# Kernel tuning notes

Measured on AMD Instinct MI355X. Metric: run time of the kernel, lower is better.

The kernel has to match this reference:

```python
import jax, jax.numpy as jnp
import numpy as np

B, Q, S = 4, 16384, 4
QD = FD = HD = 256
H = W = 128
OFFSET_SCALE = 0.05


def grid_sample_bilinear(feats, grid):
    # feats [B,C,H,W], grid [B,N,2] (x,y) normalized coords, align_corners=True, zeros padding
    Bb, C, Hh, Ww = feats.shape
    x = (grid[..., 0] + 1.0) * 0.5 * (Ww - 1)
    y = (grid[..., 1] + 1.0) * 0.5 * (Hh - 1)
    x0 = jnp.floor(x)
    y0 = jnp.floor(y)
    wx1 = x - x0
    wy1 = y - y0
    x0i = x0.astype(jnp.int32)
    y0i = y0.astype(jnp.int32)
    flat = feats.reshape(Bb, C, Hh * Ww)

    def corner(xi, yi, w):
        valid = ((xi >= 0) & (xi < Ww) & (yi >= 0) & (yi < Hh)).astype(feats.dtype)
        idx = jnp.clip(yi, 0, Hh - 1) * Ww + jnp.clip(xi, 0, Ww - 1)
        vals = jnp.take_along_axis(flat, idx[:, None, :], axis=2)  # [B,C,N]
        return vals * (w * valid)[:, None, :]

    return (corner(x0i, y0i, (1 - wx1) * (1 - wy1))
            + corner(x0i + 1, y0i, wx1 * (1 - wy1))
            + corner(x0i, y0i + 1, (1 - wx1) * wy1)
            + corner(x0i + 1, y0i + 1, wx1 * wy1))  # [B,C,N]


def setup_inputs() -> dict:
    key = jax.random.key(0)
    ks = jax.random.split(key, 12)
    queries = jax.random.normal(ks[0], (B, Q, QD), jnp.float32)
    ref_points = jax.random.uniform(ks[1], (B, Q, 2), jnp.float32, -0.95, 0.95)
    feature_map = jax.random.normal(ks[2], (B, FD, H, W), jnp.float32)
    valid_mask = jax.random.randint(ks[3], (B, Q), 0, 10) > 0
    s = 0.02
    Wq = jax.random.normal(ks[4], (QD, HD), jnp.float32) * s
    bq = jnp.zeros((HD,), jnp.float32)
    Wf = jax.random.normal(ks[5], (FD, HD), jnp.float32) * s  # 1x1 conv weight
    bf = jnp.zeros((HD,), jnp.float32)
    Wo = jax.random.normal(ks[6], (QD, 2 * S), jnp.float32) * s
    bo = jnp.zeros((2 * S,), jnp.float32)
    Ww = jax.random.normal(ks[7], (QD, S), jnp.float32) * s
    bw = jnp.zeros((S,), jnp.float32)
    W1 = jax.random.normal(ks[8], (2 * HD, HD), jnp.float32) * s
    b1 = jnp.zeros((HD,), jnp.float32)
    W2 = jax.random.normal(ks[9], (HD, HD), jnp.float32) * s
    b2 = jnp.zeros((HD,), jnp.float32)
    return dict(queries=queries, ref_points=ref_points, feature_map=feature_map,
                valid_mask=valid_mask, Wq=Wq, bq=bq, Wf=Wf, bf=bf, Wo=Wo, bo=bo,
                Ww=Ww, bw=bw, W1=W1, b1=b1, W2=W2, b2=b2)


def reference(queries, ref_points, feature_map, valid_mask,
              Wq, bq, Wf, bf, Wo, bo, Ww, bw, W1, b1, W2, b2):
    Bb, Qq, _ = queries.shape
    Ss = Ww.shape[1]
    Hd = Wq.shape[1]
    pq = queries @ Wq + bq                                    # [B,Q,HD]
    pf = jnp.einsum('bchw,cd->bdhw', feature_map, Wf) + bf[None, :, None, None]
    off = jnp.tanh(queries @ Wo + bo).reshape(Bb, Qq, Ss, 2) * OFFSET_SCALE
    w = jax.nn.softmax(queries @ Ww + bw, axis=-1)            # [B,Q,S]
    grid = jnp.clip(ref_points[:, :, None, :] + off, -1.2, 1.2).reshape(Bb, Qq * Ss, 2)
    sampled = grid_sample_bilinear(pf, grid)                  # [B,HD,Q*S]
    sampled = sampled.reshape(Bb, Hd, Qq, Ss).transpose(0, 2, 3, 1)  # [B,Q,S,HD]
    m = valid_mask.astype(sampled.dtype)
    sampled = sampled * m[:, :, None, None]
    w = w * m[:, :, None]
    w = w / jnp.clip(jnp.sum(w, axis=-1, keepdims=True), 1e-6, None)
    ctx = jnp.sum(sampled * w[..., None], axis=2)             # [B,Q,HD]
    ctx = ctx * m[:, :, None]
    pq = pq * m[:, :, None]
    hcat = jnp.concatenate([pq, ctx], axis=-1)                # [B,Q,2*HD]
    return jax.nn.relu(hcat @ W1 + b1) @ W2 + b2
```

## Files before the change

kernel.cpp:

```cpp
#include <hip/hip_runtime.h>
#include <hip/hip_bf16.h>
#include <math.h>


#define NQ 65536
#define OFFSET_SCALE 0.05f

typedef __bf16 bf16x8 __attribute__((ext_vector_type(8)));
typedef float f32x4 __attribute__((ext_vector_type(4)));
typedef float f32x2 __attribute__((ext_vector_type(2)));

__device__ __forceinline__ float dot4(float4 a, float4 b) {
  return a.x * b.x + a.y * b.y + a.z * b.z + a.w * b.w;
}

__device__ __forceinline__ ushort f2bf(float f) {
  union { float f; unsigned u; } v; v.f = f;
  unsigned r = v.u + 0x7FFFu + ((v.u >> 16) & 1u);
  return (ushort)(r >> 16);
}

__device__ __forceinline__ f32x2 up2(unsigned u) {
  union { unsigned u; float f; } lo, hi;
  lo.u = u << 16;
  hi.u = u & 0xFFFF0000u;
  f32x2 r = {lo.f, hi.f};
  return r;
}

__device__ __forceinline__ unsigned pkbf(f32x2 v) {
  float2 f; f.x = v[0]; f.y = v[1];
  union { __hip_bfloat162 h; unsigned u; } x;
  x.h = __float22bfloat162_rn(f);
  return x.u;
}

__device__ __forceinline__ void gload16(const void* g, void* s) {
  __builtin_amdgcn_global_load_lds(
      (const __attribute__((address_space(1))) void*)g,
      (__attribute__((address_space(3))) void*)s, 16, 0, 0);
}

__global__ void __launch_bounds__(256) k_misc(
    const float* __restrict__ fm, ushort* __restrict__ fmT,
    const float* __restrict__ Wq, const float* __restrict__ Wf,
    const float* __restrict__ W1, const float* __restrict__ W2,
    const float* __restrict__ bq, const float* __restrict__ bf,
    ushort* __restrict__ ABt, ushort* __restrict__ W2t,
    float* __restrict__ uvec, float* __restrict__ vvec,
    const float* __restrict__ queries, const int* __restrict__ valid,
    const float* __restrict__ Wo, const float* __restrict__ bo,
    const float* __restrict__ Ww, const float* __restrict__ bw,
    float* __restrict__ proj, ushort* __restrict__ qraw) {
  __shared__ float smem[128 * 65];
  const int bid = blockIdx.x;
  const int t = threadIdx.x;

  if (bid < 2048) {
    const int c0 = (bid & 3) * 64;
    const int y  = (bid >> 2) & 127;
    const int b  = bid >> 9;
    float (*tile)[65] = (float(*)[65])smem;
    for (int idx = t; idx < 64 * 128; idx += 256) {
      const int ci = idx >> 7, x = idx & 127;
      tile[x][ci] = fm[(((size_t)(b * 256 + c0 + ci) * 128 + y) << 7) + x];
    }
    __syncthreads();
    for (int idx = t; idx < 128 * 16; idx += 256) {
      const int x = idx >> 4, cg = idx & 15;
      ushort4 o;
      o.x = f2bf(tile[x][cg * 4 + 0]);
      o.y = f2bf(tile[x][cg * 4 + 1]);
      o.z = f2bf(tile[x][cg * 4 + 2]);
      o.w = f2bf(tile[x][cg * 4 + 3]);
      *(ushort4*)(fmT + (((size_t)((b * 128 + y) * 128 + x)) << 8) + c0 + cg * 4) = o;
    }
  } else if (bid < 2817) {
    const int blk = bid - 2048;
    const int n = t;
    if (blk < 256) {
      float s = 0.f;
      for (int j = 0; j < 256; ++j) s = fmaf(Wq[blk * 256 + j], W1[j * 256 + n], s);
      ABt[(size_t)n * 512 + blk] = f2bf(s);
    } else if (blk < 512) {
      const int k = blk - 256;
      float s = 0.f;
      for (int j = 0; j < 256; ++j) s = fmaf(Wf[k * 256 + j], W1[(256 + j) * 256 + n], s);
      ABt[(size_t)n * 512 + 256 + k] = f2bf(s);
    } else if (blk == 512) {
      float su = 0.f, sv = 0.f;
      for (int j = 0; j < 256; ++j) {
        su = fmaf(bq[j], W1[j * 256 + n], su);
        sv = fmaf(bf[j], W1[(256 + j) * 256 + n], sv);
      }
      uvec[n] = su;
      vvec[n] = sv;
    } else {
      const int k = blk - 513;
      W2t[(size_t)n * 256 + k] = f2bf(W2[(size_t)k * 256 + n]);
    }
  } else {
    const int blk = bid - 2817;
    float (*sW)[260] = (float(*)[260])smem;
    float* sb = smem + 12 * 260;
    for (int i = t; i < 2048; i += 256) sW[i & 7][i >> 3] = Wo[i];
    for (int i = t; i < 1024; i += 256) sW[8 + (i & 3)][i >> 2] = Ww[i];
    if (t < 8) sb[t] = bo[t];
    else if (t < 12) sb[t] = bw[t - 8];
    __syncthreads();

    const int lane = t & 63, wv = t >> 6;
    const int ql = lane >> 4, kc = lane & 15;
    const int qi = blk * 16 + wv * 4 + ql;
    const float mf = (valid[qi] != 0) ? 1.0f : 0.0f;

    float4 qv[4];
#pragma unroll
    for (int i = 0; i < 4; ++i)
      qv[i] = *(const float4*)(queries + (size_t)qi * 256 + kc * 4 + i * 64);

    float pr[12];
#pragma unroll
    for (int j = 0; j < 12; ++j) {
      float s = 0.f;
#pragma unroll
      for (int i = 0; i < 4; ++i)
        s += dot4(qv[i], *(const float4*)&sW[j][kc * 4 + i * 64]);
      pr[j] = s;
    }
#pragma unroll
    for (int m = 1; m < 16; m <<= 1) {
#pragma unroll
      for (int j = 0; j < 12; ++j) pr[j] += __shfl_xor(pr[j], m, 64);
    }
    if (kc == 0) {
      float4* pp = (float4*)(proj + (size_t)qi * 16);
      const float4 o0 = {pr[0] + sb[0], pr[1] + sb[1], pr[2] + sb[2],  pr[3] + sb[3]};
      const float4 o1 = {pr[4] + sb[4], pr[5] + sb[5], pr[6] + sb[6],  pr[7] + sb[7]};
      const float4 o2 = {pr[8] + sb[8], pr[9] + sb[9], pr[10] + sb[10], pr[11] + sb[11]};
      pp[0] = o0; pp[1] = o1; pp[2] = o2;
    }
#pragma unroll
    for (int i = 0; i < 4; ++i) {
      ushort4 h;
      h.x = f2bf(qv[i].x * mf); h.y = f2bf(qv[i].y * mf);
      h.z = f2bf(qv[i].z * mf); h.w = f2bf(qv[i].w * mf);
      *(ushort4*)(qraw + (size_t)qi * 512 + kc * 4 + i * 64) = h;
    }
  }
}

__global__ void __launch_bounds__(256) k_gather(
    const float* __restrict__ proj, const float* __restrict__ ref,
    const int* __restrict__ valid, const ushort* __restrict__ fmT,
    ushort* __restrict__ qraw, float* __restrict__ cov) {
  const int t = threadIdx.x, lane = t & 63, wv = t >> 6;
  const int qs = lane >> 4;
  const int kc = lane & 15;
  const int xcd = blockIdx.x & 7;
  const int b = xcd >> 1;
  const int p = ((blockIdx.x >> 3) << 1) | (xcd & 1);
  const ushort* fmTb = fmT + ((size_t)b << 22);

#pragma unroll 1
  for (int it = 0; it < 2; ++it) {
    const int qi = b * 16384 + it * 8192 + p * 16 + wv * 4 + qs;
    const float mf = (valid[qi] != 0) ? 1.0f : 0.0f;
    const float4 pA = *(const float4*)(proj + (size_t)qi * 16);
    const float4 pB = *(const float4*)(proj + (size_t)qi * 16 + 4);
    const float4 pC = *(const float4*)(proj + (size_t)qi * 16 + 8);
    const float rx = ref[qi * 2], ry = ref[qi * 2 + 1];

    const float po[8] = {pA.x, pA.y, pA.z, pA.w, pB.x, pB.y, pB.z, pB.w};
    float o[8];
#pragma unroll
    for (int j = 0; j < 8; ++j) {
      const float x = po[j];
      const float e = __expf(2.0f * fabsf(x));
      const float th = 1.0f - 2.0f * __builtin_amdgcn_rcpf(e + 1.0f);
      o[j] = copysignf(th, x) * OFFSET_SCALE;
    }
    float wl[4] = {pC.x, pC.y, pC.z, pC.w};
    const float wmax = fmaxf(fmaxf(wl[0], wl[1]), fmaxf(wl[2], wl[3]));
    float wsum = 0.f;
#pragma unroll
    for (int j = 0; j < 4; ++j) { wl[j] = __expf(wl[j] - wmax); wsum += wl[j]; }
    const float winv = mf * __builtin_amdgcn_rcpf(wsum);

    f32x2 acc[8] = {};
    float cv = 0.f;

#define CORN(PIXPTR, CF)                                                     \
    do {                                                                     \
      const float cfv = (CF);                                                \
      const uint4 u0 = *(const uint4*)((PIXPTR) + kc * 8);                   \
      const uint4 u1 = *(const uint4*)((PIXPTR) + kc * 8 + 128);             \
      const f32x2 c2 = {cfv, cfv};                                           \
      acc[0] += c2 * up2(u0.x); acc[1] += c2 * up2(u0.y);                    \
      acc[2] += c2 * up2(u0.z); acc[3] += c2 * up2(u0.w);                    \
      acc[4] += c2 * up2(u1.x); acc[5] += c2 * up2(u1.y);                    \
      acc[6] += c2 * up2(u1.z); acc[7] += c2 * up2(u1.w);                    \
    } while (0)

#pragma unroll
    for (int s = 0; s < 4; ++s) {
      const float wgt = wl[s] * winv;
      const float gx = fminf(fmaxf(rx + o[2 * s],     -1.2f), 1.2f);
      const float gy = fminf(fmaxf(ry + o[2 * s + 1], -1.2f), 1.2f);
      const float xf = (gx + 1.0f) * 63.5f;
      const float yf = (gy + 1.0f) * 63.5f;
      const float x0f = floorf(xf), y0f = floorf(yf);
      const float wx = xf - x0f, wy = yf - y0f;
      const int x0 = (int)x0f, y0 = (int)y0f;
      const float wx0 = ((unsigned)x0 < 128u) ? (1.0f - wx) : 0.0f;
      const float wx1 = ((unsigned)(x0 + 1) < 128u) ? wx : 0.0f;
      const float wy0 = ((unsigned)y0 < 128u) ? (wgt * (1.0f - wy)) : 0.0f;
      const float wy1 = ((unsigned)(y0 + 1) < 128u) ? (wgt * wy) : 0.0f;
      const int xc0 = min(max(x0, 0), 127), xc1 = min(max(x0 + 1, 0), 127);
      const int yc0 = min(max(y0, 0), 127), yc1 = min(max(y0 + 1, 0), 127);
      cv += (wx0 + wx1) * (wy0 + wy1);
      const ushort* r0 = fmTb + ((size_t)yc0 << 15);
      const ushort* r1 = fmTb + ((size_t)yc1 << 15);
      CORN(r0 + (xc0 << 8), wy0 * wx0);
      CORN(r0 + (xc1 << 8), wy0 * wx1);
      CORN(r1 + (xc0 << 8), wy1 * wx0);
      CORN(r1 + (xc1 << 8), wy1 * wx1);
    }
#undef CORN

    uint4 w0, w1;
    w0.x = pkbf(acc[0]); w0.y = pkbf(acc[1]); w0.z = pkbf(acc[2]); w0.w = pkbf(acc[3]);
    w1.x = pkbf(acc[4]); w1.y = pkbf(acc[5]); w1.z = pkbf(acc[6]); w1.w = pkbf(acc[7]);
    *(uint4*)(qraw + (size_t)qi * 512 + 256 + kc * 8) = w0;
    *(uint4*)(qraw + (size_t)qi * 512 + 256 + 128 + kc * 8) = w1;
    if (kc == 0) cov[qi] = cv;
  }
}

__global__ void __launch_bounds__(256, 3) k_gemm_fused(
    const ushort* __restrict__ qraw, const ushort* __restrict__ ABt,
    const ushort* __restrict__ W2t, const int* __restrict__ valid,
    const float* __restrict__ cov, const float* __restrict__ uvec,
    const float* __restrict__ vvec, const float* __restrict__ b1,
    const float* __restrict__ b2, float* __restrict__ out) {
  __shared__ ushort As[64 * 32];
  __shared__ ushort Bs[256 * 32];
  __shared__ ushort Hs[64 * 256];
  const int t = threadIdx.x;
  const int m0 = blockIdx.x * 64;
  const int wn = t >> 6, lane = t & 63;
  const int lr = lane & 15, lg = lane >> 4;

  const int srow = t >> 2;
  const int schunk = ((t & 3) ^ ((srow >> 1) & 3)) * 8;
  const int swz = (lg ^ ((lr >> 1) & 3)) * 8;

  const ushort* ag = qraw + (size_t)(m0 + srow) * 512 + schunk;
  const ushort* bg = ABt + (size_t)srow * 512 + schunk;
  ushort* la = As + t * 8;
  ushort* lb = Bs + t * 8;

  f32x4 acc[4][4] = {};

  for (int k0 = 0; k0 < 512; k0 += 32) {
    __syncthreads();
    gload16(ag + k0, la);
    gload16(bg + k0, lb);
    gload16(bg + 64 * 512 + k0, lb + 2048);
    gload16(bg + 128 * 512 + k0, lb + 4096);
    gload16(bg + 192 * 512 + k0, lb + 6144);
    __syncthreads();
    bf16x8 af[4], bfr[4];
#pragma unroll
    for (int m = 0; m < 4; ++m)
      af[m] = *(const bf16x8*)(As + (m * 16 + lr) * 32 + swz);
#pragma unroll
    for (int n = 0; n < 4; ++n)
      bfr[n] = *(const bf16x8*)(Bs + (wn * 64 + n * 16 + lr) * 32 + swz);
#pragma unroll
    for (int m = 0; m < 4; ++m)
#pragma unroll
      for (int n = 0; n < 4; ++n)
        acc[m][n] = __builtin_amdgcn_mfma_f32_16x16x32_bf16(af[m], bfr[n], acc[m][n], 0, 0, 0);
  }

  {
    float uu[4], vv[4], bb[4];
#pragma unroll
    for (int n = 0; n < 4; ++n) {
      const int col = wn * 64 + n * 16 + lr;
      uu[n] = uvec[col]; vv[n] = vvec[col]; bb[n] = b1[col];
    }
#pragma unroll
    for (int m = 0; m < 4; ++m)
#pragma unroll
      for (int j = 0; j < 4; ++j) {
        const int row = m * 16 + lg * 4 + j;
        const float mfv = valid[m0 + row] ? 1.0f : 0.0f;
        const float cvr = cov[m0 + row];
#pragma unroll
        for (int n = 0; n < 4; ++n) {
          const int col = wn * 64 + n * 16 + lr;
          float r = acc[m][n][j] + mfv * uu[n] + cvr * vv[n] + bb[n];
          r = fmaxf(r, 0.0f);
          const int slot = (col >> 3) ^ (row & 7);
          Hs[row * 256 + slot * 8 + (col & 7)] = f2bf(r);
        }
      }
  }

  const ushort* cg = W2t + (size_t)srow * 256 + schunk;
#pragma unroll
  for (int m = 0; m < 4; ++m)
#pragma unroll
    for (int n = 0; n < 4; ++n) {
      f32x4 z = {0.f, 0.f, 0.f, 0.f};
      acc[m][n] = z;
    }

  for (int k0 = 0; k0 < 256; k0 += 32) {
    __syncthreads();
    gload16(cg + k0, lb);
    gload16(cg + 64 * 256 + k0, lb + 2048);
    gload16(cg + 128 * 256 + k0, lb + 4096);
    gload16(cg + 192 * 256 + k0, lb + 6144);
    __syncthreads();
    bf16x8 af[4], bfr[4];
#pragma unroll
    for (int m = 0; m < 4; ++m) {
      const int slot = ((k0 >> 3) + lg) ^ (lr & 7);
      af[m] = *(const bf16x8*)(Hs + (m * 16 + lr) * 256 + slot * 8);
    }
#pragma unroll
    for (int n = 0; n < 4; ++n)
      bfr[n] = *(const bf16x8*)(Bs + (wn * 64 + n * 16 + lr) * 32 + swz);
#pragma unroll
    for (int m = 0; m < 4; ++m)
#pragma unroll
      for (int n = 0; n < 4; ++n)
        acc[m][n] = __builtin_amdgcn_mfma_f32_16x16x32_bf16(af[m], bfr[n], acc[m][n], 0, 0, 0);
  }

  {
    float bb[4];
#pragma unroll
    for (int n = 0; n < 4; ++n) bb[n] = b2[wn * 64 + n * 16 + lr];
#pragma unroll
    for (int m = 0; m < 4; ++m)
#pragma unroll
      for (int j = 0; j < 4; ++j) {
        const int row = m0 + m * 16 + lg * 4 + j;
#pragma unroll
        for (int n = 0; n < 4; ++n)
          out[(size_t)row * 256 + wn * 64 + n * 16 + lr] = acc[m][n][j] + bb[n];
      }
  }
}

extern "C" void kernel_launch(void* const* d_in, const int* in_sizes, int n_in,
                              void* d_out, int out_size, void* d_ws, size_t ws_size,
                              hipStream_t stream) {
  const float* queries = (const float*)d_in[0];
  const float* ref     = (const float*)d_in[1];
  const float* fm      = (const float*)d_in[2];
  const int*   valid   = (const int*)d_in[3];
  const float* Wq = (const float*)d_in[4];
  const float* bq = (const float*)d_in[5];
  const float* Wf = (const float*)d_in[6];
  const float* bf = (const float*)d_in[7];
  const float* Wo = (const float*)d_in[8];
  const float* bo = (const float*)d_in[9];
  const float* Ww = (const float*)d_in[10];
  const float* bw = (const float*)d_in[11];
  const float* W1 = (const float*)d_in[12];
  const float* b1 = (const float*)d_in[13];
  const float* W2 = (const float*)d_in[14];
  const float* b2 = (const float*)d_in[15];
  float* out = (float*)d_out;

  char* ws = (char*)d_ws;
  ushort* qraw = (ushort*)ws;
  float*  cov  = (float*)(ws + 67108864);
  ushort* ABt  = (ushort*)(ws + 67108864 + 262144);
  ushort* W2t  = (ushort*)(ws + 67108864 + 524288);
  float*  uvec = (float*)(ws + 67108864 + 655360);
  float*  vvec = uvec + 256;

  ushort* fmT  = (ushort*)d_out;
  float*  proj = out + 9437184;

  k_misc<<<6913, 256, 0, stream>>>(fm, fmT, Wq, Wf, W1, W2, bq, bf, ABt, W2t,
                                   uvec, vvec, queries, valid, Wo, bo, Ww, bw,
                                   proj, qraw);
  k_gather<<<2048, 256, 0, stream>>>(proj, ref, valid, fmT, qraw, cov);
  k_gemm_fused<<<1024, 256, 0, stream>>>(qraw, ABt, W2t, valid, cov, uvec, vvec,
                                         b1, b2, out);
}
```

Before: 136.2 us.

## Fuse query offset/weight projection into gather kernel and store bf16 transpose tile

Moves the per-query Wo/Ww projection and the bf16 copy of the queries out of k_misc and into k_gather. The projection results no longer go through a global proj buffer and are consumed directly in registers, which removes one write-plus-read round trip and 4096 blocks from k_misc. The feature-map transpose tile is now stored as bf16 in LDS, converted before the write, with the loops fully unrolled. The W1 precompute loops use four independent accumulators. In exchange, every gather block must load Wo/Ww into LDS and read the queries before sampling, which lengthens the gather critical path and raises its LDS use.

```diff
diff --git a/kernel.cpp b/kernel.cpp
--- a/kernel.cpp
+++ b/kernel.cpp
@@ -47,12 +47,8 @@
     const float* __restrict__ W1, const float* __restrict__ W2,
     const float* __restrict__ bq, const float* __restrict__ bf,
     ushort* __restrict__ ABt, ushort* __restrict__ W2t,
-    float* __restrict__ uvec, float* __restrict__ vvec,
-    const float* __restrict__ queries, const int* __restrict__ valid,
-    const float* __restrict__ Wo, const float* __restrict__ bo,
-    const float* __restrict__ Ww, const float* __restrict__ bw,
-    float* __restrict__ proj, ushort* __restrict__ qraw) {
-  __shared__ float smem[128 * 65];
+    float* __restrict__ uvec, float* __restrict__ vvec) {
+  __shared__ ushort tile[128][70];
   const int bid = blockIdx.x;
   const int t = threadIdx.x;
 
@@ -60,35 +56,47 @@
     const int c0 = (bid & 3) * 64;
     const int y  = (bid >> 2) & 127;
     const int b  = bid >> 9;
-    float (*tile)[65] = (float(*)[65])smem;
-    for (int idx = t; idx < 64 * 128; idx += 256) {
+#pragma unroll
+    for (int rep = 0; rep < 32; ++rep) {
+      const int idx = t + rep * 256;
       const int ci = idx >> 7, x = idx & 127;
-      tile[x][ci] = fm[(((size_t)(b * 256 + c0 + ci) * 128 + y) << 7) + x];
-    }
-    __syncthreads();
-    for (int idx = t; idx < 128 * 16; idx += 256) {
+      tile[x][ci] = f2bf(fm[(((size_t)(b * 256 + c0 + ci) * 128 + y) << 7) + x]);
+    }
+    __syncthreads();
+#pragma unroll
+    for (int rep = 0; rep < 8; ++rep) {
+      const int idx = t + rep * 256;
       const int x = idx >> 4, cg = idx & 15;
-      ushort4 o;
-      o.x = f2bf(tile[x][cg * 4 + 0]);
-      o.y = f2bf(tile[x][cg * 4 + 1]);
-      o.z = f2bf(tile[x][cg * 4 + 2]);
-      o.w = f2bf(tile[x][cg * 4 + 3]);
+      const ushort4 o = *(const ushort4*)&tile[x][cg * 4];
       *(ushort4*)(fmT + (((size_t)((b * 128 + y) * 128 + x)) << 8) + c0 + cg * 4) = o;
     }
-  } else if (bid < 2817) {
+  } else {
     const int blk = bid - 2048;
     const int n = t;
     if (blk < 256) {
-      float s = 0.f;
-      for (int j = 0; j < 256; ++j) s = fmaf(Wq[blk * 256 + j], W1[j * 256 + n], s);
-      ABt[(size_t)n * 512 + blk] = f2bf(s);
+      float s0 = 0.f, s1 = 0.f, s2 = 0.f, s3 = 0.f;
+#pragma unroll 4
+      for (int j = 0; j < 256; j += 4) {
+        s0 = fmaf(Wq[blk * 256 + j + 0], W1[(j + 0) * 256 + n], s0);
+        s1 = fmaf(Wq[blk * 256 + j + 1], W1[(j + 1) * 256 + n], s1);
+        s2 = fmaf(Wq[blk * 256 + j + 2], W1[(j + 2) * 256 + n], s2);
+        s3 = fmaf(Wq[blk * 256 + j + 3], W1[(j + 3) * 256 + n], s3);
+      }
+      ABt[(size_t)n * 512 + blk] = f2bf((s0 + s1) + (s2 + s3));
     } else if (blk < 512) {
       const int k = blk - 256;
-      float s = 0.f;
-      for (int j = 0; j < 256; ++j) s = fmaf(Wf[k * 256 + j], W1[(256 + j) * 256 + n], s);
-      ABt[(size_t)n * 512 + 256 + k] = f2bf(s);
+      float s0 = 0.f, s1 = 0.f, s2 = 0.f, s3 = 0.f;
+#pragma unroll 4
+      for (int j = 0; j < 256; j += 4) {
+        s0 = fmaf(Wf[k * 256 + j + 0], W1[(256 + j + 0) * 256 + n], s0);
+        s1 = fmaf(Wf[k * 256 + j + 1], W1[(256 + j + 1) * 256 + n], s1);
+        s2 = fmaf(Wf[k * 256 + j + 2], W1[(256 + j + 2) * 256 + n], s2);
+        s3 = fmaf(Wf[k * 256 + j + 3], W1[(256 + j + 3) * 256 + n], s3);
+      }
+      ABt[(size_t)n * 512 + 256 + k] = f2bf((s0 + s1) + (s2 + s3));
     } else if (blk == 512) {
       float su = 0.f, sv = 0.f;
+#pragma unroll 4
       for (int j = 0; j < 256; ++j) {
         su = fmaf(bq[j], W1[j * 256 + n], su);
         sv = fmaf(bf[j], W1[(256 + j) * 256 + n], sv);
@@ -99,62 +107,25 @@
       const int k = blk - 513;
       W2t[(size_t)n * 256 + k] = f2bf(W2[(size_t)k * 256 + n]);
     }
-  } else {
-    const int blk = bid - 2817;
-    float (*sW)[260] = (float(*)[260])smem;
-    float* sb = smem + 12 * 260;
-    for (int i = t; i < 2048; i += 256) sW[i & 7][i >> 3] = Wo[i];
-    for (int i = t; i < 1024; i += 256) sW[8 + (i & 3)][i >> 2] = Ww[i];
-    if (t < 8) sb[t] = bo[t];
-    else if (t < 12) sb[t] = bw[t - 8];
-    __syncthreads();
-
-    const int lane = t & 63, wv = t >> 6;
-    const int ql = lane >> 4, kc = lane & 15;
-    const int qi = blk * 16 + wv * 4 + ql;
-    const float mf = (valid[qi] != 0) ? 1.0f : 0.0f;
-
-    float4 qv[4];
-#pragma unroll
-    for (int i = 0; i < 4; ++i)
-      qv[i] = *(const float4*)(queries + (size_t)qi * 256 + kc * 4 + i * 64);
-
-    float pr[12];
-#pragma unroll
-    for (int j = 0; j < 12; ++j) {
-      float s = 0.f;
-#pragma unroll
-      for (int i = 0; i < 4; ++i)
-        s += dot4(qv[i], *(const float4*)&sW[j][kc * 4 + i * 64]);
-      pr[j] = s;
-    }
-#pragma unroll
-    for (int m = 1; m < 16; m <<= 1) {
-#pragma unroll
-      for (int j = 0; j < 12; ++j) pr[j] += __shfl_xor(pr[j], m, 64);
-    }
-    if (kc == 0) {
-      float4* pp = (float4*)(proj + (size_t)qi * 16);
-      const float4 o0 = {pr[0] + sb[0], pr[1] + sb[1], pr[2] + sb[2],  pr[3] + sb[3]};
-      const float4 o1 = {pr[4] + sb[4], pr[5] + sb[5], pr[6] + sb[6],  pr[7] + sb[7]};
-      const float4 o2 = {pr[8] + sb[8], pr[9] + sb[9], pr[10] + sb[10], pr[11] + sb[11]};
-      pp[0] = o0; pp[1] = o1; pp[2] = o2;
-    }
-#pragma unroll
-    for (int i = 0; i < 4; ++i) {
-      ushort4 h;
-      h.x = f2bf(qv[i].x * mf); h.y = f2bf(qv[i].y * mf);
-      h.z = f2bf(qv[i].z * mf); h.w = f2bf(qv[i].w * mf);
-      *(ushort4*)(qraw + (size_t)qi * 512 + kc * 4 + i * 64) = h;
-    }
   }
 }
 
 __global__ void __launch_bounds__(256) k_gather(
-    const float* __restrict__ proj, const float* __restrict__ ref,
-    const int* __restrict__ valid, const ushort* __restrict__ fmT,
+    const float* __restrict__ queries, const float* __restrict__ ref,
+    const int* __restrict__ valid, const float* __restrict__ Wo,
+    const float* __restrict__ bo, const float* __restrict__ Ww,
+    const float* __restrict__ bw, const ushort* __restrict__ fmT,
     ushort* __restrict__ qraw, float* __restrict__ cov) {
-  const int t = threadIdx.x, lane = t & 63, wv = t >> 6;
+  __shared__ float sW[12][260];
+  __shared__ float sb[12];
+  const int t = threadIdx.x;
+  for (int i = t; i < 2048; i += 256) sW[i & 7][i >> 3] = Wo[i];
+  for (int i = t; i < 1024; i += 256) sW[8 + (i & 3)][i >> 2] = Ww[i];
+  if (t < 8) sb[t] = bo[t];
+  else if (t < 12) sb[t] = bw[t - 8];
+  __syncthreads();
+
+  const int lane = t & 63, wv = t >> 6;
   const int qs = lane >> 4;
   const int kc = lane & 15;
   const int xcd = blockIdx.x & 7;
@@ -166,26 +137,50 @@
   for (int it = 0; it < 2; ++it) {
     const int qi = b * 16384 + it * 8192 + p * 16 + wv * 4 + qs;
     const float mf = (valid[qi] != 0) ? 1.0f : 0.0f;
-    const float4 pA = *(const float4*)(proj + (size_t)qi * 16);
-    const float4 pB = *(const float4*)(proj + (size_t)qi * 16 + 4);
-    const float4 pC = *(const float4*)(proj + (size_t)qi * 16 + 8);
-    const float rx = ref[qi * 2], ry = ref[qi * 2 + 1];
-
-    const float po[8] = {pA.x, pA.y, pA.z, pA.w, pB.x, pB.y, pB.z, pB.w};
+
+    float4 qv[4];
+#pragma unroll
+    for (int i = 0; i < 4; ++i)
+      qv[i] = *(const float4*)(queries + (size_t)qi * 256 + kc * 4 + i * 64);
+#pragma unroll
+    for (int i = 0; i < 4; ++i) {
+      ushort4 h;
+      h.x = f2bf(qv[i].x * mf); h.y = f2bf(qv[i].y * mf);
+      h.z = f2bf(qv[i].z * mf); h.w = f2bf(qv[i].w * mf);
+      *(ushort4*)(qraw + (size_t)qi * 512 + kc * 4 + i * 64) = h;
+    }
+    float pr[12];
+#pragma unroll
+    for (int j = 0; j < 12; ++j) {
+      float s = 0.f;
+#pragma unroll
+      for (int i = 0; i < 4; ++i)
+        s += dot4(qv[i], *(const float4*)&sW[j][kc * 4 + i * 64]);
+      pr[j] = s;
+    }
+#pragma unroll
+    for (int m = 1; m < 16; m <<= 1) {
+#pragma unroll
+      for (int j = 0; j < 12; ++j) pr[j] += __shfl_xor(pr[j], m, 64);
+    }
+
     float o[8];
 #pragma unroll
     for (int j = 0; j < 8; ++j) {
-      const float x = po[j];
+      const float x = pr[j] + sb[j];
       const float e = __expf(2.0f * fabsf(x));
       const float th = 1.0f - 2.0f * __builtin_amdgcn_rcpf(e + 1.0f);
       o[j] = copysignf(th, x) * OFFSET_SCALE;
     }
-    float wl[4] = {pC.x, pC.y, pC.z, pC.w};
+    float wl[4];
+#pragma unroll
+    for (int j = 0; j < 4; ++j) wl[j] = pr[8 + j] + sb[8 + j];
     const float wmax = fmaxf(fmaxf(wl[0], wl[1]), fmaxf(wl[2], wl[3]));
     float wsum = 0.f;
 #pragma unroll
     for (int j = 0; j < 4; ++j) { wl[j] = __expf(wl[j] - wmax); wsum += wl[j]; }
     const float winv = mf * __builtin_amdgcn_rcpf(wsum);
+    const float rx = ref[qi * 2], ry = ref[qi * 2 + 1];
 
     f32x2 acc[8] = {};
     float cv = 0.f;
@@ -387,12 +382,11 @@
   float*  vvec = uvec + 256;
 
   ushort* fmT  = (ushort*)d_out;
-  float*  proj = out + 9437184;
-
-  k_misc<<<6913, 256, 0, stream>>>(fm, fmT, Wq, Wf, W1, W2, bq, bf, ABt, W2t,
-                                   uvec, vvec, queries, valid, Wo, bo, Ww, bw,
-                                   proj, qraw);
-  k_gather<<<2048, 256, 0, stream>>>(proj, ref, valid, fmT, qraw, cov);
+
+  k_misc<<<2817, 256, 0, stream>>>(fm, fmT, Wq, Wf, W1, W2, bq, bf, ABt, W2t,
+                                   uvec, vvec);
+  k_gather<<<2048, 256, 0, stream>>>(queries, ref, valid, Wo, bo, Ww, bw, fmT,
+                                     qraw, cov);
   k_gemm_fused<<<1024, 256, 0, stream>>>(qraw, ABt, W2t, valid, cov, uvec, vvec,
                                          b1, b2, out);
 }
```

Result: slower. 255.9 us (+87.8%).
